# Optimization experiments

Measured on AMD Instinct MI355X. Metric: run time of the kernel, lower is better.

## Reference

```python
import jax, jax.numpy as jnp
import numpy as np
from functools import partial

B, W, D = 512, 64, 512          # batch, window, latent_dim
H = 1024                        # hidden_dim
N, K, C = 1024, 8, 64           # codebook_size, codes_per_step, code_dim
BN = K * C                      # bottleneck dim = 512
COMMIT_W = 0.25


def setup_inputs() -> dict:
    key = jax.random.key(0)
    ks = jax.random.split(key, 16)
    s = 0.02
    return {
        "state_window": jax.random.normal(ks[0], (B, W, D), jnp.float32),
        # GRU params (PyTorch layout: [3H, in] with gate order r, z, n)
        "W_ih": jax.random.normal(ks[1], (3 * H, D), jnp.float32) * s,
        "W_hh": jax.random.normal(ks[2], (3 * H, H), jnp.float32) * s,
        "b_ih": jax.random.normal(ks[3], (3 * H,), jnp.float32) * s,
        "b_hh": jax.random.normal(ks[4], (3 * H,), jnp.float32) * s,
        # query projection
        "Wq": jax.random.normal(ks[5], (K * C, H), jnp.float32) * s,
        "bq": jnp.zeros((K * C,), jnp.float32),
        # codebook
        "emb": jax.random.normal(ks[6], (N, C), jnp.float32) * s,
        # uncertainty head: Linear(D+BN -> H), SiLU, Linear(H -> H)
        "uW1": jax.random.normal(ks[7], (H, D + BN), jnp.float32) * s,
        "ub1": jnp.zeros((H,), jnp.float32),
        "uW2": jax.random.normal(ks[8], (H, H), jnp.float32) * s,
        "ub2": jnp.zeros((H,), jnp.float32),
        # self-prediction head: Linear(BN -> H), SiLU, Linear(H -> BN)
        "pW1": jax.random.normal(ks[9], (H, BN), jnp.float32) * s,
        "pb1": jnp.zeros((H,), jnp.float32),
        "pW2": jax.random.normal(ks[10], (BN, H), jnp.float32) * s,
        "pb2": jnp.zeros((BN,), jnp.float32),
    }


def _gru(x_seq, W_ih, W_hh, b_ih, b_hh):
    """x_seq: [B, W, D] -> final hidden [B, H] (PyTorch GRU equations)."""
    # precompute input projections for all timesteps: [W, B, 3H]
    gi_all = jnp.einsum('bwd,gd->wbg', x_seq, W_ih) + b_ih

    def step(h, gi):
        gh = h @ W_hh.T + b_hh
        i_r, i_z, i_n = jnp.split(gi, 3, axis=-1)
        h_r, h_z, h_n = jnp.split(gh, 3, axis=-1)
        r = jax.nn.sigmoid(i_r + h_r)
        z = jax.nn.sigmoid(i_z + h_z)
        n = jnp.tanh(i_n + r * h_n)
        h = (1.0 - z) * n + z * h
        return h, None

    h0 = jnp.zeros((x_seq.shape[0], W_hh.shape[1]), x_seq.dtype)
    hT, _ = jax.lax.scan(step, h0, gi_all)
    return hT


def reference(state_window, W_ih, W_hh, b_ih, b_hh, Wq, bq, emb,
              uW1, ub1, uW2, ub2, pW1, pb1, pW2, pb2):
    sg = jax.lax.stop_gradient
    last_hidden = _gru(state_window, W_ih, W_hh, b_ih, b_hh)      # [B, H]

    queries = (last_hidden @ Wq.T + bq).reshape(-1, K, C)          # [B, K, C]

    # VQ: pairwise squared distances to codebook [B, K, N]
    d = (jnp.sum(queries ** 2, axis=-1, keepdims=True)
         + jnp.sum(emb ** 2, axis=-1)[None, None, :]
         - 2.0 * jnp.einsum('bkc,nc->bkn', queries, emb))
    code_indices = jnp.argmin(d, axis=-1)                          # [B, K] int
    quantized = emb[code_indices]                                  # [B, K, C]

    commit_loss = jnp.mean((sg(queries) - quantized) ** 2)
    codebook_loss = jnp.mean((queries - sg(quantized)) ** 2)
    vq_loss = codebook_loss + COMMIT_W * commit_loss
    quantized_st = queries + sg(quantized - queries)               # straight-through

    narrator_state = quantized_st.reshape(quantized_st.shape[0], -1)  # [B, K*C]
    last_world_state = state_window[:, -1]                            # [B, D]

    u_in = jnp.concatenate([last_world_state, narrator_state], axis=-1)
    uncertainty = jax.nn.silu(u_in @ uW1.T + ub1) @ uW2.T + ub2       # [B, H]
    predicted_next_state = jax.nn.silu(narrator_state @ pW1.T + pb1) @ pW2.T + pb2  # [B, K*C]

    return (code_indices, quantized_st, narrator_state, uncertainty,
            predicted_next_state, vq_loss, last_hidden)
```

## Files before the change

kernel.cpp:

```cpp
#include <hip/hip_runtime.h>
#include <math.h>

#define B_ 512
#define W_ 64
#define D_ 512
#define H_ 1024
#define NC_ 1024
#define K_ 8
#define C_ 64
#define BN_ 512
#define G3 (3*H_)

typedef unsigned short u16;
typedef __attribute__((ext_vector_type(8))) short bf16x8;
typedef __attribute__((ext_vector_type(4))) float f32x4;

__device__ __forceinline__ float bf_up(u16 h) { return __uint_as_float(((unsigned)h) << 16); }
__device__ __forceinline__ u16 bf_rn(float x) {
    unsigned u = __float_as_uint(x);
    return (u16)((u + 0x7FFFu + ((u >> 16) & 1u)) >> 16);
}

__device__ __forceinline__ void split8v(float4 x, float4 y, uint4& H, uint4& L) {
    float v[8] = {x.x, x.y, x.z, x.w, y.x, y.y, y.z, y.w};
    union { u16 s[8]; uint4 u; } Hh, Ll;
    #pragma unroll
    for (int i = 0; i < 8; ++i) {
        unsigned ub = __float_as_uint(v[i]);
        u16 hi = (u16)(ub >> 16);
        Hh.s[i] = hi;
        Ll.s[i] = bf_rn(v[i] - bf_up(hi));
    }
    H = Hh.u; L = Ll.u;
}

__device__ __forceinline__ void cvt_store8(u16* ph, u16* pl, float4 x, float4 y) {
    uint4 H, L; split8v(x, y, H, L);
    *(uint4*)ph = H;
    *(uint4*)pl = L;
}

struct GArgs {
    const float* A;  long lda;
    const float* Bw;
    const u16* Bhi;  const u16* Blo;
    const float* bias;
    float* C;  long ldc;
    int K;
};

template<int ACT, int BPRE>
__device__ __forceinline__ void gemm_core64(const GArgs g, int bx, int by, u16* lds)
{
    u16* Ah = lds;
    u16* Al = lds + 2560;
    u16* Bh = lds + 5120;
    u16* Bl = lds + 7680;
    const int tid = threadIdx.x;
    const int l = tid & 63, wv = tid >> 6;
    const int m0 = by * 64, n0 = bx * 64;
    const int sr = tid >> 2, sc = (tid & 3) * 8;
    const int sA = sr * 40 + sc;

    const float* Ap = g.A + (long)(m0 + sr) * g.lda + sc;
    const float* Bp = 0; const u16 *Bph = 0, *Bpl = 0;
    if (BPRE) { Bph = g.Bhi + (long)(n0 + sr) * g.K + sc; Bpl = g.Blo + (long)(n0 + sr) * g.K + sc; }
    else      { Bp  = g.Bw  + (long)(n0 + sr) * g.K + sc; }

    f32x4 acc[4] = {};

    for (int k0 = 0; k0 < g.K; k0 += 32) {
        float4 a0 = *(const float4*)(Ap + k0);
        float4 a1 = *(const float4*)(Ap + k0 + 4);
        float4 b0, b1; uint4 h0, l0;
        if (BPRE) { h0 = *(const uint4*)(Bph + k0); l0 = *(const uint4*)(Bpl + k0); }
        else      { b0 = *(const float4*)(Bp + k0); b1 = *(const float4*)(Bp + k0 + 4); }
        __syncthreads();
        cvt_store8(Ah + sA, Al + sA, a0, a1);
        if (BPRE) { *(uint4*)(Bh + sA) = h0; *(uint4*)(Bl + sA) = l0; }
        else      { cvt_store8(Bh + sA, Bl + sA, b0, b1); }
        __syncthreads();

        const int fr = (l & 15) * 40 + (l >> 4) * 8;
        bf16x8 bh = *(const bf16x8*)(Bh + wv * 640 + fr);
        bf16x8 bl = *(const bf16x8*)(Bl + wv * 640 + fr);
        #pragma unroll
        for (int mt = 0; mt < 4; ++mt) {
            bf16x8 ah = *(const bf16x8*)(Ah + mt * 640 + fr);
            bf16x8 al = *(const bf16x8*)(Al + mt * 640 + fr);
            acc[mt] = __builtin_amdgcn_mfma_f32_16x16x32_bf16(ah, bh, acc[mt], 0, 0, 0);
            acc[mt] = __builtin_amdgcn_mfma_f32_16x16x32_bf16(ah, bl, acc[mt], 0, 0, 0);
            acc[mt] = __builtin_amdgcn_mfma_f32_16x16x32_bf16(al, bh, acc[mt], 0, 0, 0);
        }
    }

    const int n = n0 + wv * 16 + (l & 15);
    const float bv = g.bias[n];
    #pragma unroll
    for (int mt = 0; mt < 4; ++mt) {
        #pragma unroll
        for (int r = 0; r < 4; ++r) {
            int m = m0 + mt * 16 + (l >> 4) * 4 + r;
            float v = acc[mt][r] + bv;
            if (ACT == 1) v = v / (1.f + expf(-v));
            g.C[(long)m * g.ldc + n] = v;
        }
    }
}

template<int ACT, int BPRE>
__global__ __launch_bounds__(256)
void hilo_gemm64(GArgs g) {
    __shared__ u16 lds[10240];
    gemm_core64<ACT, BPRE>(g, blockIdx.x, blockIdx.y, lds);
}

struct FS2 {
    const u16* hAh; const u16* hAl;
    const float* h_in; float* h_out;
    u16* hOh; u16* hOl;
    const u16* WFh; const u16* WFl;
    const float* b_hh;
    const float* gi_in;
    const u16* xh; const u16* xl;
    const u16* XFh; const u16* XFl;
    const float* b_ih;
    float* gi_out;
    const float* xpack_src;
    u16* xph; u16* xpl;
    int do_gi;
};

template<int NKC, int EPI>
__device__ __forceinline__ void step_core(const FS2& f, int bx, int by, u16* lds)
{
    const int tid = threadIdx.x, l = tid & 63, wv = tid >> 6;
    const int mh = wv & 1, nh = wv >> 1;
    const int m0 = by * 64;
    const int lda = NKC * 32;

    const u16 *Ah_g, *Al_g, *BFh, *BFl;
    if (EPI == 0) { Ah_g = f.hAh; Al_g = f.hAl; BFh = f.WFh; BFl = f.WFl; }
    else          { Ah_g = f.xh;  Al_g = f.xl;  BFh = f.XFh; BFl = f.XFl; }

    const int row = tid >> 2, c8 = (tid & 3) * 8;
    const u16* pAh = Ah_g + (long)(m0 + row) * lda + c8;
    const u16* pAl = Al_g + (long)(m0 + row) * lda + c8;
    const int sOff = row * 40 + c8;

    const int nfb = bx * 6 + nh * 3;
    const u16* pBh[3]; const u16* pBl[3];
    #pragma unroll
    for (int g = 0; g < 3; ++g) {
        long o = (((long)(nfb + g) * NKC) * 64 + l) * 8;
        pBh[g] = BFh + o; pBl[g] = BFl + o;
    }

    uint4 sa, sl;
    uint4 bhC[3], blC[3], bhN[3], blN[3];

    #define LDA_(kc) { sa = *(const uint4*)(pAh + (kc)*32); sl = *(const uint4*)(pAl + (kc)*32); }
    #define WRA_(bi) { u16* bb = lds + (bi)*5120; *(uint4*)(bb + sOff) = sa; *(uint4*)(bb + 2560 + sOff) = sl; }
    #define LDB_(kc, BH, BL) { long ko = (long)(kc)*512; \
        BH[0] = *(const uint4*)(pBh[0]+ko); BH[1] = *(const uint4*)(pBh[1]+ko); BH[2] = *(const uint4*)(pBh[2]+ko); \
        BL[0] = *(const uint4*)(pBl[0]+ko); BL[1] = *(const uint4*)(pBl[1]+ko); BL[2] = *(const uint4*)(pBl[2]+ko); }

    f32x4 acc[2][3] = {};
    const int frA = (mh * 32 + (l & 15)) * 40 + (l >> 4) * 8;

    LDA_(0); WRA_(0); LDB_(0, bhC, blC);
    for (int kc = 0; kc < NKC; ++kc) {
        const bool more = (kc + 1 < NKC);
        if (more) { LDA_(kc + 1); LDB_(kc + 1, bhN, blN); }
        __syncthreads();
        u16* buf = lds + (kc & 1) * 5120;
        bf16x8 a_h[2], a_l[2];
        #pragma unroll
        for (int mt = 0; mt < 2; ++mt) {
            a_h[mt] = *(const bf16x8*)(buf + frA + mt * 640);
            a_l[mt] = *(const bf16x8*)(buf + 2560 + frA + mt * 640);
        }
        #pragma unroll
        for (int g = 0; g < 3; ++g) {
            bf16x8 bh = *(const bf16x8*)&bhC[g];
            bf16x8 bl = *(const bf16x8*)&blC[g];
            #pragma unroll
            for (int mt = 0; mt < 2; ++mt) {
                acc[mt][g] = __builtin_amdgcn_mfma_f32_16x16x32_bf16(a_h[mt], bh, acc[mt][g], 0, 0, 0);
                acc[mt][g] = __builtin_amdgcn_mfma_f32_16x16x32_bf16(a_h[mt], bl, acc[mt][g], 0, 0, 0);
                acc[mt][g] = __builtin_amdgcn_mfma_f32_16x16x32_bf16(a_l[mt], bh, acc[mt][g], 0, 0, 0);
            }
        }
        if (more) {
            WRA_((kc + 1) & 1);
            #pragma unroll
            for (int g = 0; g < 3; ++g) { bhC[g] = bhN[g]; blC[g] = blN[g]; }
        }
    }
    #undef LDA_
    #undef WRA_
    #undef LDB_

    if (EPI == 0) {
        const int j = (bx * 2 + nh) * 16 + (l & 15);
        const float bhr = f.b_hh[j], bhz = f.b_hh[H_ + j], bhn = f.b_hh[2 * H_ + j];
        #pragma unroll
        for (int mt = 0; mt < 2; ++mt) {
            #pragma unroll
            for (int r = 0; r < 4; ++r) {
                int m = m0 + mh * 32 + mt * 16 + (l >> 4) * 4 + r;
                const float* gib = f.gi_in + (long)m * G3;
                float ir = gib[j], iz = gib[H_ + j], inn = gib[2 * H_ + j];
                float hr = acc[mt][0][r] + bhr;
                float hz = acc[mt][1][r] + bhz;
                float hn = acc[mt][2][r] + bhn;
                float rg = 1.f / (1.f + expf(-(ir + hr)));
                float zg = 1.f / (1.f + expf(-(iz + hz)));
                float ng = tanhf(inn + rg * hn);
                float hv = (1.f - zg) * ng + zg * f.h_in[(long)m * H_ + j];
                long oidx = (long)m * H_ + j;
                f.h_out[oidx] = hv;
                unsigned ub = __float_as_uint(hv);
                u16 hh = (u16)(ub >> 16);
                f.hOh[oidx] = hh;
                f.hOl[oidx] = bf_rn(hv - bf_up(hh));
            }
        }
    } else {
        #pragma unroll
        for (int g = 0; g < 3; ++g) {
            const int n = (nfb + g) * 16 + (l & 15);
            const float bv = f.b_ih[n];
            #pragma unroll
            for (int mt = 0; mt < 2; ++mt) {
                #pragma unroll
                for (int r = 0; r < 4; ++r) {
                    int m = m0 + mh * 32 + mt * 16 + (l >> 4) * 4 + r;
                    f.gi_out[(long)m * G3 + n] = acc[mt][g][r] + bv;
                }
            }
        }
    }
}

__device__ __forceinline__ void pack_slice_dev(const float* src, u16* dh, u16* dl,
                                               int blk, int tid)
{
    #pragma unroll
    for (int it = 0; it < 16; ++it) {
        int e4 = blk * 4096 + it * 256 + tid;
        int b = e4 >> 7, dd = (e4 & 127) * 4;
        float4 v = *(const float4*)(src + (long)b * (W_ * D_) + dd);
        union { u16 s[4]; uint2 u; } Hh, Ll;
        float vv[4] = {v.x, v.y, v.z, v.w};
        #pragma unroll
        for (int i = 0; i < 4; ++i) {
            unsigned ub = __float_as_uint(vv[i]);
            u16 hi = (u16)(ub >> 16);
            Hh.s[i] = hi;
            Ll.s[i] = bf_rn(vv[i] - bf_up(hi));
        }
        long o = (long)b * D_ + dd;
        *(uint2*)(dh + o) = Hh.u;
        *(uint2*)(dl + o) = Ll.u;
    }
}

__global__ __launch_bounds__(256)
void gru_fused2(FS2 f)
{
    __shared__ u16 lds[10240];
    const int id = blockIdx.x;
    if (id < 256) {
        step_core<32, 0>(f, id & 31, id >> 5, lds);
    } else if (id < 512) {
        if (!f.do_gi) return;
        int id2 = id - 256;
        step_core<16, 1>(f, id2 & 31, id2 >> 5, lds);
    } else {
        if (!f.xpack_src) return;
        pack_slice_dev(f.xpack_src, f.xph, f.xpl, id - 512, threadIdx.x);
    }
}

__global__ __launch_bounds__(256)
void gi_init(FS2 f)
{
    __shared__ u16 lds[10240];
    step_core<16, 1>(f, blockIdx.x & 31, blockIdx.x >> 5, lds);
}

__global__ __launch_bounds__(256)
void pack_x(const float* src, u16* dh, u16* dl)
{
    pack_slice_dev(src, dh, dl, blockIdx.x, threadIdx.x);
}

__global__ __launch_bounds__(256)
void to_hilo(const float* __restrict__ src, u16* __restrict__ hi, u16* __restrict__ lo, long n8) {
    long i = (long)blockIdx.x * 256 + threadIdx.x;
    if (i >= n8) return;
    float4 a = ((const float4*)src)[2 * i];
    float4 b = ((const float4*)src)[2 * i + 1];
    uint4 H, L; split8v(a, b, H, L);
    ((uint4*)hi)[i] = H;
    ((uint4*)lo)[i] = L;
}

__global__ __launch_bounds__(256)
void prep_whh(const float* __restrict__ W, u16* __restrict__ fh, u16* __restrict__ fl)
{
    long t = (long)blockIdx.x * 256 + threadIdx.x;
    if (t >= (long)192 * 32 * 64) return;
    int l = (int)(t & 63);
    long nk = t >> 6;
    int kc = (int)(nk & 31);
    int nf = (int)(nk >> 5);
    int p = nf * 16 + (l & 15);
    int jg = p / 48, g = (p % 48) >> 4, jl = p & 15;
    int srow = g * H_ + jg * 16 + jl;
    int k0 = kc * 32 + (l >> 4) * 8;
    float4 v0 = *(const float4*)(W + (long)srow * H_ + k0);
    float4 v1 = *(const float4*)(W + (long)srow * H_ + k0 + 4);
    uint4 H, L; split8v(v0, v1, H, L);
    ((uint4*)fh)[t] = H;
    ((uint4*)fl)[t] = L;
}

__global__ __launch_bounds__(256)
void prep_wih(const float* __restrict__ W, u16* __restrict__ fh, u16* __restrict__ fl)
{
    long t = (long)blockIdx.x * 256 + threadIdx.x;
    if (t >= (long)192 * 16 * 64) return;
    int l = (int)(t & 63);
    long nk = t >> 6;
    int kc = (int)(nk & 15);
    int nf = (int)(nk >> 4);
    int srow = nf * 16 + (l & 15);
    int k0 = kc * 32 + (l >> 4) * 8;
    float4 v0 = *(const float4*)(W + (long)srow * D_ + k0);
    float4 v1 = *(const float4*)(W + (long)srow * D_ + k0 + 4);
    uint4 H, L; split8v(v0, v1, H, L);
    ((uint4*)fh)[t] = H;
    ((uint4*)fl)[t] = L;
}

struct StepArgs {
    const float* h_in;  float* h_out;
    const float* W_hh;
    const float* gi;
    const float* b_hh;
    const float* xw;
    const float* W_ih;
    const float* b_ih;
    float* gi_out;
};

__global__ __launch_bounds__(256)
void gru_step2(StepArgs s)
{
    __shared__ u16 lds[17920];
    const int id = blockIdx.x;
    const int tid = threadIdx.x;
    if (id >= 256) {
        if (!s.xw) return;
        int id2 = id - 256;
        GArgs g;
        g.A = s.xw; g.lda = (long)W_ * D_;
        g.Bw = s.W_ih; g.Bhi = 0; g.Blo = 0;
        g.bias = s.b_ih; g.C = s.gi_out; g.ldc = G3; g.K = D_;
        gemm_core64<0, 0>(g, id2 % 48, id2 / 48, lds);
        return;
    }
    u16* Ah = lds;
    u16* Al = lds + 1280;
    u16* Bh = lds + 2560;
    u16* Bl = lds + 10240;
    const int by = id >> 4, bx = id & 15;
    const int l = tid & 63, wv = tid >> 6;
    const int m0 = by * 32, j0 = bx * 64;
    const int sr = tid >> 2, sc = (tid & 3) * 8;
    const int sA = sr * 40 + sc;

    const float* Ap = s.h_in + (long)(m0 + (tid >> 2)) * H_ + sc;

    f32x4 acc[2][3] = {};

    for (int k0 = 0; k0 < H_; k0 += 32) {
        float4 a0, a1;
        if (tid < 128) {
            a0 = *(const float4*)(Ap + k0);
            a1 = *(const float4*)(Ap + k0 + 4);
        }
        float4 bf0[3], bf1[3];
        #pragma unroll
        for (int g = 0; g < 3; ++g) {
            long rowp = (long)(g * H_ + j0 + sr);
            bf0[g] = *(const float4*)(s.W_hh + rowp * H_ + k0 + sc);
            bf1[g] = *(const float4*)(s.W_hh + rowp * H_ + k0 + sc + 4);
        }
        __syncthreads();
        if (tid < 128) cvt_store8(Ah + sA, Al + sA, a0, a1);
        #pragma unroll
        for (int g = 0; g < 3; ++g)
            cvt_store8(Bh + g * 2560 + sA, Bl + g * 2560 + sA, bf0[g], bf1[g]);
        __syncthreads();

        const int fr = (l & 15) * 40 + (l >> 4) * 8;
        bf16x8 bhf[3], blf[3];
        #pragma unroll
        for (int g = 0; g < 3; ++g) {
            bhf[g] = *(const bf16x8*)(Bh + g * 2560 + wv * 640 + fr);
            blf[g] = *(const bf16x8*)(Bl + g * 2560 + wv * 640 + fr);
        }
        #pragma unroll
        for (int mt = 0; mt < 2; ++mt) {
            bf16x8 ah = *(const bf16x8*)(Ah + mt * 640 + fr);
            bf16x8 al = *(const bf16x8*)(Al + mt * 640 + fr);
            #pragma unroll
            for (int g = 0; g < 3; ++g) {
                acc[mt][g] = __builtin_amdgcn_mfma_f32_16x16x32_bf16(ah, bhf[g], acc[mt][g], 0, 0, 0);
                acc[mt][g] = __builtin_amdgcn_mfma_f32_16x16x32_bf16(ah, blf[g], acc[mt][g], 0, 0, 0);
                acc[mt][g] = __builtin_amdgcn_mfma_f32_16x16x32_bf16(al, bhf[g], acc[mt][g], 0, 0, 0);
            }
        }
    }

    const int j = j0 + wv * 16 + (l & 15);
    const float bhr = s.b_hh[j], bhz = s.b_hh[H_ + j], bhn = s.b_hh[2 * H_ + j];
    #pragma unroll
    for (int mt = 0; mt < 2; ++mt) {
        #pragma unroll
        for (int r = 0; r < 4; ++r) {
            int m = m0 + mt * 16 + (l >> 4) * 4 + r;
            const float* gib = s.gi + (long)m * G3;
            float ir = gib[j], iz = gib[H_ + j], inn = gib[2 * H_ + j];
            float hr = acc[mt][0][r] + bhr;
            float hz = acc[mt][1][r] + bhz;
            float hn = acc[mt][2][r] + bhn;
            float rg = 1.f / (1.f + expf(-(ir + hr)));
            float zg = 1.f / (1.f + expf(-(iz + hz)));
            float ng = tanhf(inn + rg * hn);
            s.h_out[(long)m * H_ + j] = (1.f - zg) * ng + zg * s.h_in[(long)m * H_ + j];
        }
    }
}

__global__ void emb_norm(const float* __restrict__ emb, float* __restrict__ e2,
                         float* __restrict__ loss_slot)
{
    int n = blockIdx.x * 256 + threadIdx.x;
    if (n == 0) *loss_slot = 0.f;
    if (n < NC_) {
        const float4* e4 = (const float4*)(emb + (long)n * C_);
        float s = 0.f;
        #pragma unroll
        for (int c = 0; c < 16; ++c) { float4 e = e4[c]; s += e.x*e.x + e.y*e.y + e.z*e.z + e.w*e.w; }
        e2[n] = s;
    }
}

__global__ __launch_bounds__(256)
void vq16(const float* __restrict__ q, const float* __restrict__ emb,
          const float* __restrict__ e2, float* __restrict__ out_f,
          int* __restrict__ out_i)
{
    __shared__ float es[128 * 68];
    const int blk = blockIdx.x, tid = threadIdx.x;
    const int qg = tid >> 4, sI = tid & 15;
    float4 qr[16];
    {
        const float4* qrow = (const float4*)(q + (long)(blk * 16 + qg) * C_);
        #pragma unroll
        for (int i = 0; i < 16; ++i) qr[i] = qrow[i];
    }
    float bestv = 3.4e38f; int besti = 0;

    for (int n0 = 0; n0 < NC_; n0 += 128) {
        __syncthreads();
        const float4* e4 = (const float4*)(emb + (long)n0 * C_);
        #pragma unroll
        for (int i = tid; i < 2048; i += 256) {
            int code = i >> 4, c4 = i & 15;
            *(float4*)(es + code * 68 + c4 * 4) = e4[i];
        }
        __syncthreads();
        #pragma unroll
        for (int jj = 0; jj < 8; ++jj) {
            int code = sI + 16 * jj;
            const float* er = es + code * 68;
            float dot = 0.f;
            #pragma unroll
            for (int c4 = 0; c4 < 16; ++c4) {
                float4 ev = *(const float4*)(er + c4 * 4);
                dot += ev.x * qr[c4].x + ev.y * qr[c4].y + ev.z * qr[c4].z + ev.w * qr[c4].w;
            }
            float d = e2[n0 + code] - 2.f * dot;
            if (d < bestv) { bestv = d; besti = n0 + code; }
        }
    }
    #pragma unroll
    for (int m = 1; m <= 8; m <<= 1) {
        float ov = __shfl_xor(bestv, m);
        int   oi = __shfl_xor(besti, m);
        if (ov < bestv || (ov == bestv && oi < besti)) { bestv = ov; besti = oi; }
    }
    if (sI == 0) {
        int bk = blk * 16 + qg;
        out_f[bk] = (float)besti;
        out_i[bk] = besti;
    }
}

__global__ __launch_bounds__(256)
void gather_loss(const float* __restrict__ q, const float* __restrict__ emb,
                 const int* __restrict__ idx, float* __restrict__ quant_out,
                 float* __restrict__ narr_out, float* __restrict__ loss_slot)
{
    int i = blockIdx.x * 256 + threadIdx.x;
    int bk = i >> 6;
    int c  = i & 63;
    float e  = emb[(long)idx[bk] * C_ + c];
    float qv = q[i];
    quant_out[i] = e;
    narr_out[i]  = e;
    float dsq = (qv - e) * (qv - e);
    __shared__ float red[256];
    red[threadIdx.x] = dsq;
    __syncthreads();
    for (int s = 128; s > 0; s >>= 1) {
        if (threadIdx.x < s) red[threadIdx.x] += red[threadIdx.x + s];
        __syncthreads();
    }
    if (threadIdx.x == 0)
        atomicAdd(loss_slot, red[0] * (1.25f / (float)(B_ * K_ * C_)));
}

__global__ __launch_bounds__(256)
void build_uin(const float* __restrict__ x, const float* __restrict__ narr,
               float* __restrict__ uin)
{
    int i = blockIdx.x * 256 + threadIdx.x;
    int b = i >> 10;
    int j = i & 1023;
    uin[i] = (j < D_) ? x[(long)b * W_ * D_ + (long)(W_ - 1) * D_ + j]
                      : narr[(long)b * BN_ + (j - D_)];
}

__global__ __launch_bounds__(256)
void copy_f(const float* __restrict__ src, float* __restrict__ dst)
{
    int i = blockIdx.x * 256 + threadIdx.x;
    dst[i] = src[i];
}

extern "C" void kernel_launch(void* const* d_in, const int* in_sizes, int n_in,
                              void* d_out, int out_size, void* d_ws, size_t ws_size,
                              hipStream_t stream)
{
    (void)in_sizes; (void)n_in; (void)out_size;
    const float* x     = (const float*)d_in[0];
    const float* W_ih  = (const float*)d_in[1];
    const float* W_hh  = (const float*)d_in[2];
    const float* b_ih  = (const float*)d_in[3];
    const float* b_hh  = (const float*)d_in[4];
    const float* Wq    = (const float*)d_in[5];
    const float* bq    = (const float*)d_in[6];
    const float* emb   = (const float*)d_in[7];
    const float* uW1   = (const float*)d_in[8];
    const float* ub1   = (const float*)d_in[9];
    const float* uW2   = (const float*)d_in[10];
    const float* ub2   = (const float*)d_in[11];
    const float* pW1   = (const float*)d_in[12];
    const float* pb1   = (const float*)d_in[13];
    const float* pW2   = (const float*)d_in[14];
    const float* pb2   = (const float*)d_in[15];

    float* ws = (float*)d_ws;
    float* hA   = ws;
    float* giA  = ws + 524288;
    float* giB  = ws + 2097152;
    float* q    = ws + 3670016;
    float* e2   = ws + 3932160;
    int*   idxi = (int*)(ws + 3933184);
    const long FLOAT_WORDS = 3937280;
    float* uin  = giB;
    float* mlph = giB + 524288;
    float* t1   = giA;

    u16* wsu = (u16*)((char*)d_ws + FLOAT_WORDS * sizeof(float));
    u16* whhF_h = wsu;             u16* whhF_l = wsu + 3145728;
    u16* wihF_h = wsu + 6291456;   u16* wihF_l = wsu + 7864320;
    u16* wqR_h  = wsu + 9437184;   u16* wqR_l  = wsu + 9961472;
    u16* uw1R_h = wsu + 10485760;  u16* uw1R_l = wsu + 11534336;
    u16* uw2R_h = wsu + 12582912;  u16* uw2R_l = wsu + 13631488;
    u16* pw1R_h = wsu + 14680064;  u16* pw1R_l = wsu + 15204352;
    u16* pw2R_h = wsu + 15728640;  u16* pw2R_l = wsu + 16252928;
    u16* hh_hi[2] = { wsu + 16777216, wsu + 17301504 };
    u16* hh_lo[2] = { wsu + 17825792, wsu + 18350080 };
    u16* xp_h[2]  = { wsu + 18874368, wsu + 19136512 };
    u16* xp_l[2]  = { wsu + 19398656, wsu + 19660800 };
    const size_t NEED_NEW = FLOAT_WORDS * sizeof(float) + (size_t)19922944 * 2;
    const bool fast = ws_size >= NEED_NEW;

    float* out = (float*)d_out;
    const long o_idx   = 0;
    const long o_quant = o_idx   + (long)B_ * K_;
    const long o_narr  = o_quant + (long)B_ * K_ * C_;
    const long o_unc   = o_narr  + (long)B_ * BN_;
    const long o_pred  = o_unc   + (long)B_ * H_;
    const long o_loss  = o_pred  + (long)B_ * BN_;
    const long o_lh    = o_loss  + 1;

    float* hB = out + o_unc;
    float* hbuf[2] = { hA, hB };
    float* gibuf[2] = { giA, giB };

    hipMemsetAsync(hA, 0, (size_t)B_ * H_ * sizeof(float), stream);
    emb_norm<<<4, 256, 0, stream>>>(emb, e2, out + o_loss);

    auto mkargs = [&](const float* A, long lda, const float* Bw, const u16* Bh, const u16* Bl,
                      const float* bias, float* C, long ldc, int Kd) {
        GArgs g; g.A = A; g.lda = lda; g.Bw = Bw; g.Bhi = Bh; g.Blo = Bl;
        g.bias = bias; g.C = C; g.ldc = ldc; g.K = Kd; return g;
    };
    auto cvt = [&](const float* s, u16* hi, u16* lo, long n) {
        long n8 = n / 8;
        to_hilo<<<(int)((n8 + 255) / 256), 256, 0, stream>>>(s, hi, lo, n8);
    };

    if (fast) {
        hipMemsetAsync(hh_hi[0], 0, (size_t)B_ * H_ * sizeof(u16), stream);
        hipMemsetAsync(hh_lo[0], 0, (size_t)B_ * H_ * sizeof(u16), stream);
        prep_whh<<<1536, 256, 0, stream>>>(W_hh, whhF_h, whhF_l);
        prep_wih<<<768, 256, 0, stream>>>(W_ih, wihF_h, wihF_l);
        cvt(Wq,  wqR_h,  wqR_l,  (long)BN_ * H_);
        cvt(uW1, uw1R_h, uw1R_l, (long)H_ * (D_ + BN_));
        cvt(uW2, uw2R_h, uw2R_l, (long)H_ * H_);
        cvt(pW1, pw1R_h, pw1R_l, (long)H_ * BN_);
        cvt(pW2, pw2R_h, pw2R_l, (long)BN_ * H_);
        pack_x<<<16, 256, 0, stream>>>(x, xp_h[0], xp_l[0]);
        pack_x<<<16, 256, 0, stream>>>(x + (long)1 * D_, xp_h[1], xp_l[1]);

        {
            FS2 f = {};
            f.xh = xp_h[0]; f.xl = xp_l[0];
            f.XFh = wihF_h; f.XFl = wihF_l;
            f.b_ih = b_ih; f.gi_out = gibuf[0];
            gi_init<<<256, 256, 0, stream>>>(f);
        }

        for (int w = 0; w < W_; ++w) {
            FS2 f;
            f.hAh = hh_hi[w & 1]; f.hAl = hh_lo[w & 1];
            f.h_in = hbuf[w & 1]; f.h_out = hbuf[(w + 1) & 1];
            f.hOh = hh_hi[(w + 1) & 1]; f.hOl = hh_lo[(w + 1) & 1];
            f.WFh = whhF_h; f.WFl = whhF_l;
            f.b_hh = b_hh;
            f.gi_in = gibuf[w & 1];
            f.xh = xp_h[(w + 1) & 1]; f.xl = xp_l[(w + 1) & 1];
            f.XFh = wihF_h; f.XFl = wihF_l;
            f.b_ih = b_ih;
            f.gi_out = gibuf[(w + 1) & 1];
            f.xpack_src = (w + 2 < W_) ? (x + (long)(w + 2) * D_) : nullptr;
            f.xph = xp_h[w & 1]; f.xpl = xp_l[w & 1];
            f.do_gi = (w + 1 < W_);
            gru_fused2<<<528, 256, 0, stream>>>(f);
        }
        float* hfin = hbuf[0];

        auto gemm = [&](int act, GArgs g, int N, int M) {
            dim3 grid(N / 64, M / 64);
            if (act == 1) hilo_gemm64<1, 1><<<grid, 256, 0, stream>>>(g);
            else          hilo_gemm64<0, 1><<<grid, 256, 0, stream>>>(g);
        };
        gemm(0, mkargs(hfin, H_, Wq, wqR_h, wqR_l, bq, q, BN_, H_), BN_, B_);
        vq16<<<256, 256, 0, stream>>>(q, emb, e2, out + o_idx, idxi);
        gather_loss<<<(B_ * K_ * C_) / 256, 256, 0, stream>>>(
            q, emb, idxi, out + o_quant, out + o_narr, out + o_loss);
        build_uin<<<(B_ * (D_ + BN_)) / 256, 256, 0, stream>>>(x, out + o_narr, uin);
        gemm(1, mkargs(uin, D_ + BN_, uW1, uw1R_h, uw1R_l, ub1, mlph, H_, D_ + BN_), H_, B_);
        gemm(0, mkargs(mlph, H_, uW2, uw2R_h, uw2R_l, ub2, out + o_unc, H_, H_), H_, B_);
        gemm(1, mkargs(out + o_narr, BN_, pW1, pw1R_h, pw1R_l, pb1, t1, H_, BN_), H_, B_);
        gemm(0, mkargs(t1, H_, pW2, pw2R_h, pw2R_l, pb2, out + o_pred, BN_, H_), BN_, B_);
        copy_f<<<(B_ * H_) / 256, 256, 0, stream>>>(hfin, out + o_lh);
        return;
    }

    {
        GArgs g0 = mkargs(x, (long)W_ * D_, W_ih, 0, 0, b_ih, gibuf[0], G3, D_);
        hilo_gemm64<0, 0><<<dim3(48, 8), 256, 0, stream>>>(g0);
    }
    for (int w = 0; w < W_; ++w) {
        StepArgs s;
        s.h_in  = hbuf[w & 1];
        s.h_out = hbuf[(w + 1) & 1];
        s.W_hh = W_hh;
        s.gi = gibuf[w & 1];
        s.b_hh = b_hh;
        s.xw = (w + 1 < W_) ? (x + (long)(w + 1) * D_) : nullptr;
        s.W_ih = W_ih;
        s.b_ih = b_ih;
        s.gi_out = gibuf[(w + 1) & 1];
        gru_step2<<<640, 256, 0, stream>>>(s);
    }
    float* hfin = hbuf[0];

    auto gemmL = [&](int act, GArgs g, int N, int M) {
        dim3 grid(N / 64, M / 64);
        if (act == 1) hilo_gemm64<1, 0><<<grid, 256, 0, stream>>>(g);
        else          hilo_gemm64<0, 0><<<grid, 256, 0, stream>>>(g);
    };
    gemmL(0, mkargs(hfin, H_, Wq, 0, 0, bq, q, BN_, H_), BN_, B_);
    vq16<<<256, 256, 0, stream>>>(q, emb, e2, out + o_idx, idxi);
    gather_loss<<<(B_ * K_ * C_) / 256, 256, 0, stream>>>(
        q, emb, idxi, out + o_quant, out + o_narr, out + o_loss);
    build_uin<<<(B_ * (D_ + BN_)) / 256, 256, 0, stream>>>(x, out + o_narr, uin);
    gemmL(1, mkargs(uin, D_ + BN_, uW1, 0, 0, ub1, mlph, H_, D_ + BN_), H_, B_);
    gemmL(0, mkargs(mlph, H_, uW2, 0, 0, ub2, out + o_unc, H_, H_), H_, B_);
    gemmL(1, mkargs(out + o_narr, BN_, pW1, 0, 0, pb1, t1, H_, BN_), H_, B_);
    gemmL(0, mkargs(t1, H_, pW2, 0, 0, pb2, out + o_pred, BN_, H_), BN_, B_);
    copy_f<<<(B_ * H_) / 256, 256, 0, stream>>>(hfin, out + o_lh);
}
```

Before: 1.905 ms.

## Store GRU hidden and input activations in MFMA fragment layout, drop LDS staging

The GRU step kernel now writes the hidden state's hi/lo bf16 split, and the packed input slices, straight into the per-lane MFMA fragment order. Each wave can then load its A operands directly from global memory into registers. This removes the LDS double buffer and the per-k-chunk __syncthreads, and the k loop is fully unrolled with two register stages of prefetch. In exchange, A tiles are no longer shared across waves through LDS, so each wave reads them from global/L2 itself. The epilogue's scattered 2-byte fragment stores and the higher register pressure could offset the gains.

```diff
diff --git a/kernel.cpp b/kernel.cpp
--- a/kernel.cpp
+++ b/kernel.cpp
@@ -115,97 +115,104 @@
     gemm_core64<ACT, BPRE>(g, blockIdx.x, blockIdx.y, lds);
 }
 
-struct FS2 {
-    const u16* hAh; const u16* hAl;
+struct FS3 {
+    const u16* hFh_in; const u16* hFl_in;
     const float* h_in; float* h_out;
-    u16* hOh; u16* hOl;
+    u16* hFh_out; u16* hFl_out;
     const u16* WFh; const u16* WFl;
     const float* b_hh;
     const float* gi_in;
-    const u16* xh; const u16* xl;
+    const u16* xFh; const u16* xFl;
     const u16* XFh; const u16* XFl;
     const float* b_ih;
     float* gi_out;
     const float* xpack_src;
-    u16* xph; u16* xpl;
+    u16* xpFh; u16* xpFl;
     int do_gi;
 };
 
+#define LD_(kc, AH0,AL0,AH1,AL1, BH0,BH1,BH2, BL0,BL1,BL2) do { long ko = (long)(kc) * 512; \
+    AH0 = *(const uint4*)(pA0h + ko); AL0 = *(const uint4*)(pA0l + ko); \
+    AH1 = *(const uint4*)(pA1h + ko); AL1 = *(const uint4*)(pA1l + ko); \
+    BH0 = *(const uint4*)(pB0h + ko); BH1 = *(const uint4*)(pB1h + ko); BH2 = *(const uint4*)(pB2h + ko); \
+    BL0 = *(const uint4*)(pB0l + ko); BL1 = *(const uint4*)(pB1l + ko); BL2 = *(const uint4*)(pB2l + ko); } while (0)
+
+#define MMA_(AH0,AL0,AH1,AL1, BH0,BH1,BH2, BL0,BL1,BL2) do { \
+    bf16x8 ah0 = *(const bf16x8*)&AH0, al0 = *(const bf16x8*)&AL0; \
+    bf16x8 ah1 = *(const bf16x8*)&AH1, al1 = *(const bf16x8*)&AL1; \
+    bf16x8 bh0 = *(const bf16x8*)&BH0, bh1 = *(const bf16x8*)&BH1, bh2 = *(const bf16x8*)&BH2; \
+    bf16x8 bl0 = *(const bf16x8*)&BL0, bl1 = *(const bf16x8*)&BL1, bl2 = *(const bf16x8*)&BL2; \
+    acc[0][0] = __builtin_amdgcn_mfma_f32_16x16x32_bf16(ah0, bh0, acc[0][0], 0, 0, 0); \
+    acc[0][0] = __builtin_amdgcn_mfma_f32_16x16x32_bf16(ah0, bl0, acc[0][0], 0, 0, 0); \
+    acc[0][0] = __builtin_amdgcn_mfma_f32_16x16x32_bf16(al0, bh0, acc[0][0], 0, 0, 0); \
+    acc[0][1] = __builtin_amdgcn_mfma_f32_16x16x32_bf16(ah0, bh1, acc[0][1], 0, 0, 0); \
+    acc[0][1] = __builtin_amdgcn_mfma_f32_16x16x32_bf16(ah0, bl1, acc[0][1], 0, 0, 0); \
+    acc[0][1] = __builtin_amdgcn_mfma_f32_16x16x32_bf16(al0, bh1, acc[0][1], 0, 0, 0); \
+    acc[0][2] = __builtin_amdgcn_mfma_f32_16x16x32_bf16(ah0, bh2, acc[0][2], 0, 0, 0); \
+    acc[0][2] = __builtin_amdgcn_mfma_f32_16x16x32_bf16(ah0, bl2, acc[0][2], 0, 0, 0); \
+    acc[0][2] = __builtin_amdgcn_mfma_f32_16x16x32_bf16(al0, bh2, acc[0][2], 0, 0, 0); \
+    acc[1][0] = __builtin_amdgcn_mfma_f32_16x16x32_bf16(ah1, bh0, acc[1][0], 0, 0, 0); \
+    acc[1][0] = __builtin_amdgcn_mfma_f32_16x16x32_bf16(ah1, bl0, acc[1][0], 0, 0, 0); \
+    acc[1][0] = __builtin_amdgcn_mfma_f32_16x16x32_bf16(al1, bh0, acc[1][0], 0, 0, 0); \
+    acc[1][1] = __builtin_amdgcn_mfma_f32_16x16x32_bf16(ah1, bh1, acc[1][1], 0, 0, 0); \
+    acc[1][1] = __builtin_amdgcn_mfma_f32_16x16x32_bf16(ah1, bl1, acc[1][1], 0, 0, 0); \
+    acc[1][1] = __builtin_amdgcn_mfma_f32_16x16x32_bf16(al1, bh1, acc[1][1], 0, 0, 0); \
+    acc[1][2] = __builtin_amdgcn_mfma_f32_16x16x32_bf16(ah1, bh2, acc[1][2], 0, 0, 0); \
+    acc[1][2] = __builtin_amdgcn_mfma_f32_16x16x32_bf16(ah1, bl2, acc[1][2], 0, 0, 0); \
+    acc[1][2] = __builtin_amdgcn_mfma_f32_16x16x32_bf16(al1, bh2, acc[1][2], 0, 0, 0); } while (0)
+
 template<int NKC, int EPI>
-__device__ __forceinline__ void step_core(const FS2& f, int bx, int by, u16* lds)
+__device__ __forceinline__ void step_core_reg(const FS3& f, int bx, int by)
 {
     const int tid = threadIdx.x, l = tid & 63, wv = tid >> 6;
     const int mh = wv & 1, nh = wv >> 1;
+    const int mfBase = by * 4 + mh * 2;
+
+    const u16 *AFh, *AFl, *BFh, *BFl;
+    if (EPI == 0) { AFh = f.hFh_in; AFl = f.hFl_in; BFh = f.WFh; BFl = f.WFl; }
+    else          { AFh = f.xFh;    AFl = f.xFl;    BFh = f.XFh; BFl = f.XFl; }
+
+    const u16* pA0h = AFh + ((long)(mfBase + 0) * NKC * 64 + l) * 8;
+    const u16* pA1h = AFh + ((long)(mfBase + 1) * NKC * 64 + l) * 8;
+    const u16* pA0l = AFl + ((long)(mfBase + 0) * NKC * 64 + l) * 8;
+    const u16* pA1l = AFl + ((long)(mfBase + 1) * NKC * 64 + l) * 8;
+
+    const int nfb = bx * 6 + nh * 3;
+    const u16* pB0h = BFh + ((long)(nfb + 0) * NKC * 64 + l) * 8;
+    const u16* pB1h = BFh + ((long)(nfb + 1) * NKC * 64 + l) * 8;
+    const u16* pB2h = BFh + ((long)(nfb + 2) * NKC * 64 + l) * 8;
+    const u16* pB0l = BFl + ((long)(nfb + 0) * NKC * 64 + l) * 8;
+    const u16* pB1l = BFl + ((long)(nfb + 1) * NKC * 64 + l) * 8;
+    const u16* pB2l = BFl + ((long)(nfb + 2) * NKC * 64 + l) * 8;
+
+    f32x4 acc[2][3] = {};
+
+    uint4 sA0h, sA0l, sA1h, sA1l, sB0h, sB1h, sB2h, sB0l, sB1l, sB2l;
+    uint4 tA0h, tA0l, tA1h, tA1l, tB0h, tB1h, tB2h, tB0l, tB1l, tB2l;
+
+    LD_(0, sA0h, sA0l, sA1h, sA1l, sB0h, sB1h, sB2h, sB0l, sB1l, sB2l);
+    LD_(1, tA0h, tA0l, tA1h, tA1l, tB0h, tB1h, tB2h, tB0l, tB1l, tB2l);
+    #pragma unroll
+    for (int kc = 0; kc < NKC; kc += 2) {
+        MMA_(sA0h, sA0l, sA1h, sA1l, sB0h, sB1h, sB2h, sB0l, sB1l, sB2l);
+        if (kc + 2 < NKC)
+            LD_(kc + 2, sA0h, sA0l, sA1h, sA1l, sB0h, sB1h, sB2h, sB0l, sB1l, sB2l);
+        MMA_(tA0h, tA0l, tA1h, tA1l, tB0h, tB1h, tB2h, tB0l, tB1l, tB2l);
+        if (kc + 3 < NKC)
+            LD_(kc + 3, tA0h, tA0l, tA1h, tA1l, tB0h, tB1h, tB2h, tB0l, tB1l, tB2l);
+    }
+
     const int m0 = by * 64;
-    const int lda = NKC * 32;
-
-    const u16 *Ah_g, *Al_g, *BFh, *BFl;
-    if (EPI == 0) { Ah_g = f.hAh; Al_g = f.hAl; BFh = f.WFh; BFl = f.WFl; }
-    else          { Ah_g = f.xh;  Al_g = f.xl;  BFh = f.XFh; BFl = f.XFl; }
-
-    const int row = tid >> 2, c8 = (tid & 3) * 8;
-    const u16* pAh = Ah_g + (long)(m0 + row) * lda + c8;
-    const u16* pAl = Al_g + (long)(m0 + row) * lda + c8;
-    const int sOff = row * 40 + c8;
-
-    const int nfb = bx * 6 + nh * 3;
-    const u16* pBh[3]; const u16* pBl[3];
-    #pragma unroll
-    for (int g = 0; g < 3; ++g) {
-        long o = (((long)(nfb + g) * NKC) * 64 + l) * 8;
-        pBh[g] = BFh + o; pBl[g] = BFl + o;
-    }
-
-    uint4 sa, sl;
-    uint4 bhC[3], blC[3], bhN[3], blN[3];
-
-    #define LDA_(kc) { sa = *(const uint4*)(pAh + (kc)*32); sl = *(const uint4*)(pAl + (kc)*32); }
-    #define WRA_(bi) { u16* bb = lds + (bi)*5120; *(uint4*)(bb + sOff) = sa; *(uint4*)(bb + 2560 + sOff) = sl; }
-    #define LDB_(kc, BH, BL) { long ko = (long)(kc)*512; \
-        BH[0] = *(const uint4*)(pBh[0]+ko); BH[1] = *(const uint4*)(pBh[1]+ko); BH[2] = *(const uint4*)(pBh[2]+ko); \
-        BL[0] = *(const uint4*)(pBl[0]+ko); BL[1] = *(const uint4*)(pBl[1]+ko); BL[2] = *(const uint4*)(pBl[2]+ko); }
-
-    f32x4 acc[2][3] = {};
-    const int frA = (mh * 32 + (l & 15)) * 40 + (l >> 4) * 8;
-
-    LDA_(0); WRA_(0); LDB_(0, bhC, blC);
-    for (int kc = 0; kc < NKC; ++kc) {
-        const bool more = (kc + 1 < NKC);
-        if (more) { LDA_(kc + 1); LDB_(kc + 1, bhN, blN); }
-        __syncthreads();
-        u16* buf = lds + (kc & 1) * 5120;
-        bf16x8 a_h[2], a_l[2];
-        #pragma unroll
-        for (int mt = 0; mt < 2; ++mt) {
-            a_h[mt] = *(const bf16x8*)(buf + frA + mt * 640);
-            a_l[mt] = *(const bf16x8*)(buf + 2560 + frA + mt * 640);
-        }
-        #pragma unroll
-        for (int g = 0; g < 3; ++g) {
-            bf16x8 bh = *(const bf16x8*)&bhC[g];
-            bf16x8 bl = *(const bf16x8*)&blC[g];
-            #pragma unroll
-            for (int mt = 0; mt < 2; ++mt) {
-                acc[mt][g] = __builtin_amdgcn_mfma_f32_16x16x32_bf16(a_h[mt], bh, acc[mt][g], 0, 0, 0);
-                acc[mt][g] = __builtin_amdgcn_mfma_f32_16x16x32_bf16(a_h[mt], bl, acc[mt][g], 0, 0, 0);
-                acc[mt][g] = __builtin_amdgcn_mfma_f32_16x16x32_bf16(a_l[mt], bh, acc[mt][g], 0, 0, 0);
-            }
-        }
-        if (more) {
-            WRA_((kc + 1) & 1);
-            #pragma unroll
-            for (int g = 0; g < 3; ++g) { bhC[g] = bhN[g]; blC[g] = blN[g]; }
-        }
-    }
-    #undef LDA_
-    #undef WRA_
-    #undef LDB_
-
     if (EPI == 0) {
         const int j = (bx * 2 + nh) * 16 + (l & 15);
+        const int kcj = j >> 5;
+        const int laneTop = ((j >> 3) & 3) * 16;
+        const int sj = j & 7;
         const float bhr = f.b_hh[j], bhz = f.b_hh[H_ + j], bhn = f.b_hh[2 * H_ + j];
         #pragma unroll
         for (int mt = 0; mt < 2; ++mt) {
+            const int mf = mfBase + mt;
+            const long foB = ((long)(mf * 32 + kcj) * 64) * 8 + sj;
             #pragma unroll
             for (int r = 0; r < 4; ++r) {
                 int m = m0 + mh * 32 + mt * 16 + (l >> 4) * 4 + r;
@@ -218,12 +225,12 @@
                 float zg = 1.f / (1.f + expf(-(iz + hz)));
                 float ng = tanhf(inn + rg * hn);
                 float hv = (1.f - zg) * ng + zg * f.h_in[(long)m * H_ + j];
-                long oidx = (long)m * H_ + j;
-                f.h_out[oidx] = hv;
+                f.h_out[(long)m * H_ + j] = hv;
                 unsigned ub = __float_as_uint(hv);
                 u16 hh = (u16)(ub >> 16);
-                f.hOh[oidx] = hh;
-                f.hOl[oidx] = bf_rn(hv - bf_up(hh));
+                long fo = foB + (long)((m & 15) + laneTop) * 8;
+                f.hFh_out[fo] = hh;
+                f.hFl_out[fo] = bf_rn(hv - bf_up(hh));
             }
         }
     } else {
@@ -243,8 +250,8 @@
     }
 }
 
-__device__ __forceinline__ void pack_slice_dev(const float* src, u16* dh, u16* dl,
-                                               int blk, int tid)
+__device__ __forceinline__ void pack_slice_frag(const float* src, u16* dh, u16* dl,
+                                                int blk, int tid)
 {
     #pragma unroll
     for (int it = 0; it < 16; ++it) {
@@ -260,40 +267,40 @@
             Hh.s[i] = hi;
             Ll.s[i] = bf_rn(vv[i] - bf_up(hi));
         }
-        long o = (long)b * D_ + dd;
-        *(uint2*)(dh + o) = Hh.u;
-        *(uint2*)(dl + o) = Ll.u;
-    }
-}
-
-__global__ __launch_bounds__(256)
-void gru_fused2(FS2 f)
-{
-    __shared__ u16 lds[10240];
+        int mf = b >> 4, kc = dd >> 5;
+        int lane = (b & 15) + ((dd >> 3) & 3) * 16;
+        long fo = ((long)(mf * 16 + kc) * 64 + lane) * 8 + (dd & 7);
+        *(uint2*)(dh + fo) = Hh.u;
+        *(uint2*)(dl + fo) = Ll.u;
+    }
+}
+
+__global__ __launch_bounds__(256)
+void gru_fused3(FS3 f)
+{
     const int id = blockIdx.x;
     if (id < 256) {
-        step_core<32, 0>(f, id & 31, id >> 5, lds);
+        step_core_reg<32, 0>(f, id & 31, id >> 5);
     } else if (id < 512) {
         if (!f.do_gi) return;
         int id2 = id - 256;
-        step_core<16, 1>(f, id2 & 31, id2 >> 5, lds);
+        step_core_reg<16, 1>(f, id2 & 31, id2 >> 5);
     } else {
         if (!f.xpack_src) return;
-        pack_slice_dev(f.xpack_src, f.xph, f.xpl, id - 512, threadIdx.x);
-    }
-}
-
-__global__ __launch_bounds__(256)
-void gi_init(FS2 f)
-{
-    __shared__ u16 lds[10240];
-    step_core<16, 1>(f, blockIdx.x & 31, blockIdx.x >> 5, lds);
-}
-
-__global__ __launch_bounds__(256)
-void pack_x(const float* src, u16* dh, u16* dl)
-{
-    pack_slice_dev(src, dh, dl, blockIdx.x, threadIdx.x);
+        pack_slice_frag(f.xpack_src, f.xpFh, f.xpFl, id - 512, threadIdx.x);
+    }
+}
+
+__global__ __launch_bounds__(256)
+void gi_init3(FS3 f)
+{
+    step_core_reg<16, 1>(f, blockIdx.x & 31, blockIdx.x >> 5);
+}
+
+__global__ __launch_bounds__(256)
+void pack_xf(const float* src, u16* dh, u16* dl)
+{
+    pack_slice_frag(src, dh, dl, blockIdx.x, threadIdx.x);
 }
 
 __global__ __launch_bounds__(256)
@@ -596,10 +603,10 @@
     u16* uw2R_h = wsu + 12582912;  u16* uw2R_l = wsu + 13631488;
     u16* pw1R_h = wsu + 14680064;  u16* pw1R_l = wsu + 15204352;
     u16* pw2R_h = wsu + 15728640;  u16* pw2R_l = wsu + 16252928;
-    u16* hh_hi[2] = { wsu + 16777216, wsu + 17301504 };
-    u16* hh_lo[2] = { wsu + 17825792, wsu + 18350080 };
-    u16* xp_h[2]  = { wsu + 18874368, wsu + 19136512 };
-    u16* xp_l[2]  = { wsu + 19398656, wsu + 19660800 };
+    u16* hF_h[2] = { wsu + 16777216, wsu + 17301504 };
+    u16* hF_l[2] = { wsu + 17825792, wsu + 18350080 };
+    u16* xF_h[2] = { wsu + 18874368, wsu + 19136512 };
+    u16* xF_l[2] = { wsu + 19398656, wsu + 19660800 };
     const size_t NEED_NEW = FLOAT_WORDS * sizeof(float) + (size_t)19922944 * 2;
     const bool fast = ws_size >= NEED_NEW;
 
@@ -630,8 +637,8 @@
     };
 
     if (fast) {
-        hipMemsetAsync(hh_hi[0], 0, (size_t)B_ * H_ * sizeof(u16), stream);
-        hipMemsetAsync(hh_lo[0], 0, (size_t)B_ * H_ * sizeof(u16), stream);
+        hipMemsetAsync(hF_h[0], 0, (size_t)B_ * H_ * sizeof(u16), stream);
+        hipMemsetAsync(hF_l[0], 0, (size_t)B_ * H_ * sizeof(u16), stream);
         prep_whh<<<1536, 256, 0, stream>>>(W_hh, whhF_h, whhF_l);
         prep_wih<<<768, 256, 0, stream>>>(W_ih, wihF_h, wihF_l);
         cvt(Wq,  wqR_h,  wqR_l,  (long)BN_ * H_);
@@ -639,33 +646,33 @@
         cvt(uW2, uw2R_h, uw2R_l, (long)H_ * H_);
         cvt(pW1, pw1R_h, pw1R_l, (long)H_ * BN_);
         cvt(pW2, pw2R_h, pw2R_l, (long)BN_ * H_);
-        pack_x<<<16, 256, 0, stream>>>(x, xp_h[0], xp_l[0]);
-        pack_x<<<16, 256, 0, stream>>>(x + (long)1 * D_, xp_h[1], xp_l[1]);
+        pack_xf<<<16, 256, 0, stream>>>(x, xF_h[0], xF_l[0]);
+        pack_xf<<<16, 256, 0, stream>>>(x + (long)1 * D_, xF_h[1], xF_l[1]);
 
         {
-            FS2 f = {};
-            f.xh = xp_h[0]; f.xl = xp_l[0];
+            FS3 f = {};
+            f.xFh = xF_h[0]; f.xFl = xF_l[0];
             f.XFh = wihF_h; f.XFl = wihF_l;
             f.b_ih = b_ih; f.gi_out = gibuf[0];
-            gi_init<<<256, 256, 0, stream>>>(f);
+            gi_init3<<<256, 256, 0, stream>>>(f);
         }
 
         for (int w = 0; w < W_; ++w) {
-            FS2 f;
-            f.hAh = hh_hi[w & 1]; f.hAl = hh_lo[w & 1];
+            FS3 f;
+            f.hFh_in = hF_h[w & 1]; f.hFl_in = hF_l[w & 1];
             f.h_in = hbuf[w & 1]; f.h_out = hbuf[(w + 1) & 1];
-            f.hOh = hh_hi[(w + 1) & 1]; f.hOl = hh_lo[(w + 1) & 1];
+            f.hFh_out = hF_h[(w + 1) & 1]; f.hFl_out = hF_l[(w + 1) & 1];
             f.WFh = whhF_h; f.WFl = whhF_l;
             f.b_hh = b_hh;
             f.gi_in = gibuf[w & 1];
-            f.xh = xp_h[(w + 1) & 1]; f.xl = xp_l[(w + 1) & 1];
+            f.xFh = xF_h[(w + 1) & 1]; f.xFl = xF_l[(w + 1) & 1];
             f.XFh = wihF_h; f.XFl = wihF_l;
             f.b_ih = b_ih;
             f.gi_out = gibuf[(w + 1) & 1];
             f.xpack_src = (w + 2 < W_) ? (x + (long)(w + 2) * D_) : nullptr;
-            f.xph = xp_h[w & 1]; f.xpl = xp_l[w & 1];
+            f.xpFh = xF_h[w & 1]; f.xpFl = xF_l[w & 1];
             f.do_gi = (w + 1 < W_);
-            gru_fused2<<<528, 256, 0, stream>>>(f);
+            gru_fused3<<<528, 256, 0, stream>>>(f);
         }
         float* hfin = hbuf[0];
 
```

Result: slower. 2.792 ms (+46.6%).
